# Performance work log

Hardware: AMD Instinct MI355X
Metric: run time of the kernel (lower is better)

The kernel has to match this reference:

```python
import jax, jax.numpy as jnp
import numpy as np

B, S, D, H = 4, 1024, 1024, 16
DH = D // H
EPS = 1e-5


def setup_inputs() -> dict:
    key = jax.random.key(0)
    ks = jax.random.split(key, 8)
    return {
        "q": jax.random.normal(ks[0], (B, S, D), jnp.float32),
        "k": jax.random.normal(ks[1], (B, S, D), jnp.float32),
        "v": jax.random.normal(ks[2], (B, S, D), jnp.float32),
        "mask": jnp.ones((B, S), jnp.float32),
        "scores": jax.random.normal(ks[3], (B, H, S, S), jnp.float32),
        "W_proj": jax.random.normal(ks[4], (D, D), jnp.float32) / np.sqrt(D),
        "W_minus": jax.random.normal(ks[5], (D, 2 * D), jnp.float32) / np.sqrt(2 * D),
        "ln_w": jnp.ones((D,), jnp.float32),
        "ln_b": jnp.zeros((D,), jnp.float32),
        "c": jnp.zeros((1,), jnp.float32),
    }


def reference(q, k, v, mask, scores, W_proj, W_minus, ln_w, ln_b, c):
    # split heads: (B,S,D) -> (B,S,H,DH)
    qh = q.reshape(B, S, H, DH)
    kh = k.reshape(B, S, H, DH)
    vh = v.reshape(B, S, H, DH)
    # scaled QK^T plus learnable-scaled residual scores
    att_scores = jnp.einsum("bqhd,bkhd->bhqk", qh, kh) / np.sqrt(DH) + c[0] * scores
    # additive mask (mask is (B, kv_len))
    att_scores = att_scores - 1e8 * (1.0 - mask)[:, None, None, :]
    att = jax.nn.softmax(att_scores, axis=-1)
    ctx = jnp.einsum("bhqk,bkhd->bqhd", att, vh).reshape(B, S, D)
    # proj (bias-free linear); dropout is identity at inference
    x = ctx @ W_proj.T
    # concat -> minus linear -> LayerNorm
    cat = jnp.concatenate([q, x], axis=-1)
    y = cat @ W_minus.T
    mu = jnp.mean(y, axis=-1, keepdims=True)
    var = jnp.mean((y - mu) ** 2, axis=-1, keepdims=True)
    y = (y - mu) * jax.lax.rsqrt(var + EPS) * ln_w + ln_b
    return (y, att_scores)
```

## Files before the change

kernel.cpp:

```cpp
#include <hip/hip_runtime.h>
#include <hip/hip_bf16.h>
#include <math.h>

#define BB 4
#define SS 1024
#define DD 1024
#define HH 16
#define DHH 64
#define BHH (BB * HH)

#define LDB 88
#define LDC 68

typedef __attribute__((ext_vector_type(8))) short short8;
typedef __attribute__((ext_vector_type(4))) float f32x4;

__device__ __forceinline__ unsigned short f2bf(float x) {
  __hip_bfloat16 h = __float2bfloat16(x);
  return *reinterpret_cast<unsigned short*>(&h);
}

__device__ __forceinline__ void stageb(const unsigned short* __restrict__ src, int ld,
                                       unsigned short* __restrict__ dst, int tid) {
#pragma unroll
  for (int u = 0; u < 2; ++u) {
    int cidx = tid + 256 * u;
    int r = cidx >> 3;
    int c8 = (cidx & 7) * 8;
    float4 v = *reinterpret_cast<const float4*>(src + (size_t)r * ld + c8);
    *reinterpret_cast<float4*>(dst + r * LDB + c8) = v;
  }
}

__device__ __forceinline__ short8 ldfrag(const unsigned short* __restrict__ base,
                                         int row16, int kh, int lane) {
  const unsigned short* p = base + (size_t)(row16 + (lane & 15)) * LDB + kh + (lane >> 4) * 8;
  return *reinterpret_cast<const short8*>(p);
}

__device__ __forceinline__ void mfma_tile(const unsigned short* As, const unsigned short* Bs,
                                          int w, int lane, f32x4 acc[4]) {
#pragma unroll
  for (int kh = 0; kh < 64; kh += 32) {
    short8 b = ldfrag(Bs, w * 16, kh, lane);
#pragma unroll
    for (int mb = 0; mb < 4; ++mb) {
      short8 a = ldfrag(As, mb * 16, kh, lane);
      acc[mb] = __builtin_amdgcn_mfma_f32_16x16x32_bf16(a, b, acc[mb], 0, 0, 0);
    }
  }
}

__device__ __forceinline__ void acc_to_lds(float* Cs, const f32x4 acc[4], int w, int lane,
                                           float scale) {
  int quad = lane >> 4, col = w * 16 + (lane & 15);
#pragma unroll
  for (int mb = 0; mb < 4; ++mb)
#pragma unroll
    for (int r = 0; r < 4; ++r)
      Cs[(mb * 16 + quad * 4 + r) * LDC + col] = acc[mb][r] * scale;
}

__global__ __launch_bounds__(256) void cvt_kernel(const float* __restrict__ in,
                                                  unsigned short* __restrict__ out, int n4) {
  int i = blockIdx.x * 256 + threadIdx.x;
  if (i < n4) {
    float4 v = reinterpret_cast<const float4*>(in)[i];
    ushort4 o;
    o.x = f2bf(v.x); o.y = f2bf(v.y); o.z = f2bf(v.z); o.w = f2bf(v.w);
    reinterpret_cast<ushort4*>(out)[i] = o;
  }
}

__global__ __launch_bounds__(256) void vtrans_kernel(const float* __restrict__ v,
                                                     unsigned short* __restrict__ vT) {
  __shared__ unsigned short T[64 * LDC];
  int tid = threadIdx.x;
  int s0 = blockIdx.x * 64, bh = blockIdx.y;
  int b = bh >> 4, h = bh & 15;
#pragma unroll
  for (int u = 0; u < 4; ++u) {
    int f = tid + 256 * u;
    int r = f >> 4, c4 = (f & 15) * 4;
    float4 vv = *reinterpret_cast<const float4*>(v + ((size_t)(b * SS + s0 + r)) * DD + h * DHH + c4);
    T[(c4 + 0) * LDC + r] = f2bf(vv.x);
    T[(c4 + 1) * LDC + r] = f2bf(vv.y);
    T[(c4 + 2) * LDC + r] = f2bf(vv.z);
    T[(c4 + 3) * LDC + r] = f2bf(vv.w);
  }
  __syncthreads();
#pragma unroll
  for (int u = 0; u < 4; ++u) {
    int f = tid + 256 * u;
    int d = f >> 4, s4 = (f & 15) * 4;
    ushort4 o = *reinterpret_cast<const ushort4*>(&T[d * LDC + s4]);
    *reinterpret_cast<ushort4*>(vT + ((size_t)(bh * DHH + d)) * SS + s0 + s4) = o;
  }
}

__global__ __launch_bounds__(256) void attn_fused_kernel(
    const unsigned short* __restrict__ qb, const unsigned short* __restrict__ kb,
    const unsigned short* __restrict__ vT, const float* __restrict__ scores,
    const float* __restrict__ mask, const float* __restrict__ c,
    float* __restrict__ att, unsigned short* __restrict__ ctxb) {
  __shared__ unsigned short Ps[64 * LDB];
  __shared__ unsigned short Ks[64 * LDB];
  __shared__ unsigned short Vs[64 * LDB];
  __shared__ float Cs[64 * LDC];
  __shared__ float mrun[64], lrun[64], ascale[64];
  int tid = threadIdx.x, lane = tid & 63, w = tid >> 6;

  int flat = blockIdx.x + 16 * blockIdx.y;
  int bh = (flat & 7) * 8 + ((flat >> 3) & 7);
  int qt = flat >> 6;
  int b = bh >> 4, h = bh & 15;
  int qr0 = qt * 64;

  int r0 = tid >> 3, c80 = (tid & 7) * 8;
  int r1 = r0 + 32;
  const unsigned short* kB = kb + (size_t)b * SS * DD + h * DHH;
  const unsigned short* vB = vT + (size_t)bh * DHH * SS;
  unsigned short* KsW0 = Ks + r0 * LDB + c80;
  unsigned short* KsW1 = Ks + r1 * LDB + c80;
  unsigned short* VsW0 = Vs + r0 * LDB + c80;
  unsigned short* VsW1 = Vs + r1 * LDB + c80;

  int rowe = tid >> 4;
  int c4 = (tid & 15) * 4;
  size_t eOff = ((size_t)(bh * SS + qr0 + rowe)) * SS + c4;
  size_t mkOff = (size_t)b * SS + c4;

  stageb(qb + ((size_t)(b * SS + qr0)) * DD + h * DHH, DD, Ps, tid);
  {
    float4 k0 = *reinterpret_cast<const float4*>(kB + (size_t)r0 * DD + c80);
    float4 k1 = *reinterpret_cast<const float4*>(kB + (size_t)r1 * DD + c80);
    float4 v0 = *reinterpret_cast<const float4*>(vB + (size_t)r0 * SS + c80);
    float4 v1 = *reinterpret_cast<const float4*>(vB + (size_t)r1 * SS + c80);
    *reinterpret_cast<float4*>(KsW0) = k0;
    *reinterpret_cast<float4*>(KsW1) = k1;
    *reinterpret_cast<float4*>(VsW0) = v0;
    *reinterpret_cast<float4*>(VsW1) = v1;
  }
  if (tid < 64) { mrun[tid] = -3.0e38f; lrun[tid] = 0.0f; }

  float4 sc[4];
#pragma unroll
  for (int u2 = 0; u2 < 4; ++u2)
    sc[u2] = *reinterpret_cast<const float4*>(scores + eOff + (size_t)u2 * 16 * SS);
  float4 mk = *reinterpret_cast<const float4*>(mask + mkOff);

  __syncthreads();

  short8 qa[2][4];
#pragma unroll
  for (int kh = 0; kh < 2; ++kh)
#pragma unroll
    for (int mb = 0; mb < 4; ++mb)
      qa[kh][mb] = ldfrag(Ps, mb * 16, kh * 32, lane);

  float cc = c[0];
  f32x4 accO[4] = {};

  for (int kt = 0; kt < 16; ++kt) {
    int kr0 = kt * 64;
    float4 kn0 = {}, kn1 = {}, vn0 = {}, vn1 = {};
    if (kt < 15) {
      int kr = kr0 + 64;
      kn0 = *reinterpret_cast<const float4*>(kB + (size_t)(kr + r0) * DD + c80);
      kn1 = *reinterpret_cast<const float4*>(kB + (size_t)(kr + r1) * DD + c80);
      vn0 = *reinterpret_cast<const float4*>(vB + (size_t)r0 * SS + kr + c80);
      vn1 = *reinterpret_cast<const float4*>(vB + (size_t)r1 * SS + kr + c80);
    }

    f32x4 acc[4] = {};
    __builtin_amdgcn_s_setprio(1);
#pragma unroll
    for (int kh = 0; kh < 2; ++kh) {
      short8 bfr = ldfrag(Ks, w * 16, kh * 32, lane);
#pragma unroll
      for (int mb = 0; mb < 4; ++mb)
        acc[mb] = __builtin_amdgcn_mfma_f32_16x16x32_bf16(qa[kh][mb], bfr, acc[mb], 0, 0, 0);
    }
    __builtin_amdgcn_s_setprio(0);
    acc_to_lds(Cs, acc, w, lane, 0.125f);
    __syncthreads();

#pragma unroll
    for (int u2 = 0; u2 < 4; ++u2) {
      int row = rowe + 16 * u2;
      float4 qk = *reinterpret_cast<const float4*>(&Cs[row * LDC + c4]);
      float o0 = qk.x + cc * sc[u2].x - 1e8f * (1.0f - mk.x);
      float o1 = qk.y + cc * sc[u2].y - 1e8f * (1.0f - mk.y);
      float o2 = qk.z + cc * sc[u2].z - 1e8f * (1.0f - mk.z);
      float o3 = qk.w + cc * sc[u2].w - 1e8f * (1.0f - mk.w);
      float4 ov = {o0, o1, o2, o3};
      *reinterpret_cast<float4*>(att + eOff + (size_t)u2 * 16 * SS + kr0) = ov;
      float m = fmaxf(fmaxf(o0, o1), fmaxf(o2, o3));
#pragma unroll
      for (int off = 1; off <= 8; off <<= 1) m = fmaxf(m, __shfl_xor(m, off));
      float mo = mrun[row];
      float mn = fmaxf(mo, m);
      float e0 = __expf(o0 - mn), e1 = __expf(o1 - mn);
      float e2 = __expf(o2 - mn), e3 = __expf(o3 - mn);
      float l = e0 + e1 + e2 + e3;
#pragma unroll
      for (int off = 1; off <= 8; off <<= 1) l += __shfl_xor(l, off);
      ushort4 pv;
      pv.x = f2bf(e0); pv.y = f2bf(e1); pv.z = f2bf(e2); pv.w = f2bf(e3);
      *reinterpret_cast<ushort4*>(&Ps[row * LDB + c4]) = pv;
      if ((tid & 15) == 0) {
        float a = __expf(mo - mn);
        lrun[row] = lrun[row] * a + l;
        mrun[row] = mn;
        ascale[row] = a;
      }
    }
    if (kt < 15) {
#pragma unroll
      for (int u2 = 0; u2 < 4; ++u2)
        sc[u2] = *reinterpret_cast<const float4*>(scores + eOff + (size_t)u2 * 16 * SS + kr0 + 64);
      mk = *reinterpret_cast<const float4*>(mask + mkOff + kr0 + 64);
    }
    __syncthreads();

#pragma unroll
    for (int mb = 0; mb < 4; ++mb) {
      int rb = mb * 16 + (lane >> 4) * 4;
      accO[mb][0] *= ascale[rb + 0];
      accO[mb][1] *= ascale[rb + 1];
      accO[mb][2] *= ascale[rb + 2];
      accO[mb][3] *= ascale[rb + 3];
    }
    __builtin_amdgcn_s_setprio(1);
    mfma_tile(Ps, Vs, w, lane, accO);
    __builtin_amdgcn_s_setprio(0);
    __syncthreads();
    if (kt < 15) {
      *reinterpret_cast<float4*>(KsW0) = kn0;
      *reinterpret_cast<float4*>(KsW1) = kn1;
      *reinterpret_cast<float4*>(VsW0) = vn0;
      *reinterpret_cast<float4*>(VsW1) = vn1;
      __syncthreads();
    }
  }

#pragma unroll
  for (int mb = 0; mb < 4; ++mb) {
    int rb = mb * 16 + (lane >> 4) * 4;
    accO[mb][0] *= 1.0f / lrun[rb + 0];
    accO[mb][1] *= 1.0f / lrun[rb + 1];
    accO[mb][2] *= 1.0f / lrun[rb + 2];
    accO[mb][3] *= 1.0f / lrun[rb + 3];
  }
  acc_to_lds(Cs, accO, w, lane, 1.0f);
  __syncthreads();
#pragma unroll
  for (int u = 0; u < 4; ++u) {
    int f = tid + 256 * u;
    int row = f >> 4, cc4 = (f & 15) * 4;
    float4 vv = *reinterpret_cast<const float4*>(&Cs[row * LDC + cc4]);
    ushort4 o;
    o.x = f2bf(vv.x); o.y = f2bf(vv.y); o.z = f2bf(vv.z); o.w = f2bf(vv.w);
    *reinterpret_cast<ushort4*>(ctxb + ((size_t)(b * SS + qr0 + row)) * DD + h * DHH + cc4) = o;
  }
}

__global__ __launch_bounds__(256) void proj_mfma_kernel(
    const unsigned short* __restrict__ A, const unsigned short* __restrict__ W,
    unsigned short* __restrict__ X) {
  __shared__ unsigned short smem[2 * 64 * LDB];
  unsigned short* As = smem;
  unsigned short* Bs = smem + 64 * LDB;
  float* Cs = reinterpret_cast<float*>(smem);
  int tid = threadIdx.x, lane = tid & 63, w = tid >> 6;
  int d0 = blockIdx.x * 64, n0 = blockIdx.y * 64;
  f32x4 acc[4] = {};
  for (int kc = 0; kc < DD; kc += 64) {
    stageb(A + (size_t)n0 * DD + kc, DD, As, tid);
    stageb(W + (size_t)d0 * DD + kc, DD, Bs, tid);
    __syncthreads();
    mfma_tile(As, Bs, w, lane, acc);
    __syncthreads();
  }
  acc_to_lds(Cs, acc, w, lane, 1.0f);
  __syncthreads();
#pragma unroll
  for (int u = 0; u < 4; ++u) {
    int f = tid + 256 * u;
    int row = f >> 4, c4 = (f & 15) * 4;
    float4 vv = *reinterpret_cast<const float4*>(&Cs[row * LDC + c4]);
    ushort4 o;
    o.x = f2bf(vv.x); o.y = f2bf(vv.y); o.z = f2bf(vv.z); o.w = f2bf(vv.w);
    *reinterpret_cast<ushort4*>(X + (size_t)(n0 + row) * DD + d0 + c4) = o;
  }
}

__global__ __launch_bounds__(256) void minus_mfma_kernel(
    const unsigned short* __restrict__ qb, const unsigned short* __restrict__ xb,
    const unsigned short* __restrict__ Wm, float* __restrict__ Y) {
  __shared__ unsigned short smem[2 * 64 * LDB];
  unsigned short* As = smem;
  unsigned short* Bs = smem + 64 * LDB;
  float* Cs = reinterpret_cast<float*>(smem);
  int tid = threadIdx.x, lane = tid & 63, w = tid >> 6;
  int d0 = blockIdx.x * 64, n0 = blockIdx.y * 64;
  f32x4 acc[4] = {};
  for (int kc = 0; kc < 2 * DD; kc += 64) {
    const unsigned short* asrc = (kc < DD) ? (qb + (size_t)n0 * DD + kc)
                                           : (xb + (size_t)n0 * DD + (kc - DD));
    stageb(asrc, DD, As, tid);
    stageb(Wm + (size_t)d0 * (2 * DD) + kc, 2 * DD, Bs, tid);
    __syncthreads();
    mfma_tile(As, Bs, w, lane, acc);
    __syncthreads();
  }
  acc_to_lds(Cs, acc, w, lane, 1.0f);
  __syncthreads();
#pragma unroll
  for (int u = 0; u < 4; ++u) {
    int f = tid + 256 * u;
    int row = f >> 4, c4 = (f & 15) * 4;
    float4 vv = *reinterpret_cast<const float4*>(&Cs[row * LDC + c4]);
    *reinterpret_cast<float4*>(Y + (size_t)(n0 + row) * DD + d0 + c4) = vv;
  }
}

__global__ __launch_bounds__(256) void ln_kernel(
    float* __restrict__ Y, const float* __restrict__ w, const float* __restrict__ b) {
  __shared__ float ps[4], ps2[4];
  int row = blockIdx.x, t = threadIdx.x;
  float* rp = Y + (size_t)row * DD;
  float4 v = *reinterpret_cast<const float4*>(rp + t * 4);
  float s = v.x + v.y + v.z + v.w;
  float s2 = v.x * v.x + v.y * v.y + v.z * v.z + v.w * v.w;
#pragma unroll
  for (int o = 32; o > 0; o >>= 1) {
    s += __shfl_down(s, o);
    s2 += __shfl_down(s2, o);
  }
  if ((t & 63) == 0) { ps[t >> 6] = s; ps2[t >> 6] = s2; }
  __syncthreads();
  s = ps[0] + ps[1] + ps[2] + ps[3];
  s2 = ps2[0] + ps2[1] + ps2[2] + ps2[3];
  float mu = s * (1.0f / DD);
  float var = s2 * (1.0f / DD) - mu * mu;
  float rs = rsqrtf(var + 1e-5f);
  float4 wv = *reinterpret_cast<const float4*>(w + t * 4);
  float4 bv = *reinterpret_cast<const float4*>(b + t * 4);
  float4 ov;
  ov.x = (v.x - mu) * rs * wv.x + bv.x;
  ov.y = (v.y - mu) * rs * wv.y + bv.y;
  ov.z = (v.z - mu) * rs * wv.z + bv.z;
  ov.w = (v.w - mu) * rs * wv.w + bv.w;
  *reinterpret_cast<float4*>(rp + t * 4) = ov;
}

extern "C" void kernel_launch(void* const* d_in, const int* in_sizes, int n_in,
                              void* d_out, int out_size, void* d_ws, size_t ws_size,
                              hipStream_t stream) {
  const float* q      = (const float*)d_in[0];
  const float* k      = (const float*)d_in[1];
  const float* v      = (const float*)d_in[2];
  const float* mask   = (const float*)d_in[3];
  const float* scores = (const float*)d_in[4];
  const float* W_proj = (const float*)d_in[5];
  const float* W_minus= (const float*)d_in[6];
  const float* ln_w   = (const float*)d_in[7];
  const float* ln_b   = (const float*)d_in[8];
  const float* c      = (const float*)d_in[9];

  float* y   = (float*)d_out;
  float* att = y + (size_t)BB * SS * DD;

  const size_t MB = 1u << 20;
  char* w = (char*)d_ws;
  unsigned short* qb   = (unsigned short*)(w);
  unsigned short* kb   = (unsigned short*)(w + 8 * MB);
  unsigned short* vT   = (unsigned short*)(w + 16 * MB);
  unsigned short* Wpb  = (unsigned short*)(w + 24 * MB);
  unsigned short* Wmb  = (unsigned short*)(w + 26 * MB);
  unsigned short* ctxb = (unsigned short*)(w + 30 * MB);
  unsigned short* xb   = (unsigned short*)(w + 38 * MB);

  const int NQ = BB * SS * DD;
  cvt_kernel<<<dim3(NQ / 4 / 256), 256, 0, stream>>>(q, qb, NQ / 4);
  cvt_kernel<<<dim3(NQ / 4 / 256), 256, 0, stream>>>(k, kb, NQ / 4);
  cvt_kernel<<<dim3(DD * DD / 4 / 256), 256, 0, stream>>>(W_proj, Wpb, DD * DD / 4);
  cvt_kernel<<<dim3(2 * DD * DD / 4 / 256), 256, 0, stream>>>(W_minus, Wmb, 2 * DD * DD / 4);
  vtrans_kernel<<<dim3(16, BHH), 256, 0, stream>>>(v, vT);

  attn_fused_kernel<<<dim3(16, BHH), 256, 0, stream>>>(qb, kb, vT, scores, mask, c, att, ctxb);
  proj_mfma_kernel<<<dim3(16, 64), 256, 0, stream>>>(ctxb, Wpb, xb);
  minus_mfma_kernel<<<dim3(16, 64), 256, 0, stream>>>(qb, xb, Wmb, y);
  ln_kernel<<<dim3(BB * SS), 256, 0, stream>>>(y, ln_w, ln_b);
}
```

Measured before the change: 676.2 us.

## Load K/V MFMA fragments directly from global into registers, drop LDS staging

In the fused attention kernel each wave now loads its own K and V B-operand fragments straight from global memory into registers, with one tile of register prefetch, instead of staging K and V tiles through shared memory. This removes the Ks/Vs LDS buffers and the two barriers per key tile that guarded their refill. It also adds a launch-bounds occupancy hint of 4 blocks. In exchange there are more, less-coalesced global loads per wave (16-byte strided reads per lane), higher register pressure, and an added barrier before the final Cs reuse.

```diff
diff --git a/kernel.cpp b/kernel.cpp
--- a/kernel.cpp
+++ b/kernel.cpp
@@ -98,14 +98,12 @@
   }
 }
 
-__global__ __launch_bounds__(256) void attn_fused_kernel(
+__global__ __launch_bounds__(256, 4) void attn_fused_kernel(
     const unsigned short* __restrict__ qb, const unsigned short* __restrict__ kb,
     const unsigned short* __restrict__ vT, const float* __restrict__ scores,
     const float* __restrict__ mask, const float* __restrict__ c,
     float* __restrict__ att, unsigned short* __restrict__ ctxb) {
   __shared__ unsigned short Ps[64 * LDB];
-  __shared__ unsigned short Ks[64 * LDB];
-  __shared__ unsigned short Vs[64 * LDB];
   __shared__ float Cs[64 * LDC];
   __shared__ float mrun[64], lrun[64], ascale[64];
   int tid = threadIdx.x, lane = tid & 63, w = tid >> 6;
@@ -116,14 +114,10 @@
   int b = bh >> 4, h = bh & 15;
   int qr0 = qt * 64;
 
-  int r0 = tid >> 3, c80 = (tid & 7) * 8;
-  int r1 = r0 + 32;
-  const unsigned short* kB = kb + (size_t)b * SS * DD + h * DHH;
-  const unsigned short* vB = vT + (size_t)bh * DHH * SS;
-  unsigned short* KsW0 = Ks + r0 * LDB + c80;
-  unsigned short* KsW1 = Ks + r1 * LDB + c80;
-  unsigned short* VsW0 = Vs + r0 * LDB + c80;
-  unsigned short* VsW1 = Vs + r1 * LDB + c80;
+  const unsigned short* kF = kb + (size_t)b * SS * DD + h * DHH
+                             + (size_t)(w * 16 + (lane & 15)) * DD + (lane >> 4) * 8;
+  const unsigned short* vF = vT + (size_t)bh * DHH * SS
+                             + (size_t)(w * 16 + (lane & 15)) * SS + (lane >> 4) * 8;
 
   int rowe = tid >> 4;
   int c4 = (tid & 15) * 4;
@@ -131,17 +125,13 @@
   size_t mkOff = (size_t)b * SS + c4;
 
   stageb(qb + ((size_t)(b * SS + qr0)) * DD + h * DHH, DD, Ps, tid);
-  {
-    float4 k0 = *reinterpret_cast<const float4*>(kB + (size_t)r0 * DD + c80);
-    float4 k1 = *reinterpret_cast<const float4*>(kB + (size_t)r1 * DD + c80);
-    float4 v0 = *reinterpret_cast<const float4*>(vB + (size_t)r0 * SS + c80);
-    float4 v1 = *reinterpret_cast<const float4*>(vB + (size_t)r1 * SS + c80);
-    *reinterpret_cast<float4*>(KsW0) = k0;
-    *reinterpret_cast<float4*>(KsW1) = k1;
-    *reinterpret_cast<float4*>(VsW0) = v0;
-    *reinterpret_cast<float4*>(VsW1) = v1;
-  }
   if (tid < 64) { mrun[tid] = -3.0e38f; lrun[tid] = 0.0f; }
+
+  short8 kcur[2], vcur[2];
+  kcur[0] = *reinterpret_cast<const short8*>(kF);
+  kcur[1] = *reinterpret_cast<const short8*>(kF + 32);
+  vcur[0] = *reinterpret_cast<const short8*>(vF);
+  vcur[1] = *reinterpret_cast<const short8*>(vF + 32);
 
   float4 sc[4];
 #pragma unroll
@@ -163,24 +153,21 @@
 
   for (int kt = 0; kt < 16; ++kt) {
     int kr0 = kt * 64;
-    float4 kn0 = {}, kn1 = {}, vn0 = {}, vn1 = {};
+    short8 kn[2] = {}, vn[2] = {};
     if (kt < 15) {
-      int kr = kr0 + 64;
-      kn0 = *reinterpret_cast<const float4*>(kB + (size_t)(kr + r0) * DD + c80);
-      kn1 = *reinterpret_cast<const float4*>(kB + (size_t)(kr + r1) * DD + c80);
-      vn0 = *reinterpret_cast<const float4*>(vB + (size_t)r0 * SS + kr + c80);
-      vn1 = *reinterpret_cast<const float4*>(vB + (size_t)r1 * SS + kr + c80);
+      kn[0] = *reinterpret_cast<const short8*>(kF + (size_t)(kr0 + 64) * DD);
+      kn[1] = *reinterpret_cast<const short8*>(kF + (size_t)(kr0 + 64) * DD + 32);
+      vn[0] = *reinterpret_cast<const short8*>(vF + kr0 + 64);
+      vn[1] = *reinterpret_cast<const short8*>(vF + kr0 + 64 + 32);
     }
 
     f32x4 acc[4] = {};
     __builtin_amdgcn_s_setprio(1);
 #pragma unroll
-    for (int kh = 0; kh < 2; ++kh) {
-      short8 bfr = ldfrag(Ks, w * 16, kh * 32, lane);
+    for (int kh = 0; kh < 2; ++kh)
 #pragma unroll
       for (int mb = 0; mb < 4; ++mb)
-        acc[mb] = __builtin_amdgcn_mfma_f32_16x16x32_bf16(qa[kh][mb], bfr, acc[mb], 0, 0, 0);
-    }
+        acc[mb] = __builtin_amdgcn_mfma_f32_16x16x32_bf16(qa[kh][mb], kcur[kh], acc[mb], 0, 0, 0);
     __builtin_amdgcn_s_setprio(0);
     acc_to_lds(Cs, acc, w, lane, 0.125f);
     __syncthreads();
@@ -232,16 +219,16 @@
       accO[mb][3] *= ascale[rb + 3];
     }
     __builtin_amdgcn_s_setprio(1);
-    mfma_tile(Ps, Vs, w, lane, accO);
+#pragma unroll
+    for (int kh = 0; kh < 2; ++kh)
+#pragma unroll
+      for (int mb = 0; mb < 4; ++mb) {
+        short8 pa = ldfrag(Ps, mb * 16, kh * 32, lane);
+        accO[mb] = __builtin_amdgcn_mfma_f32_16x16x32_bf16(pa, vcur[kh], accO[mb], 0, 0, 0);
+      }
     __builtin_amdgcn_s_setprio(0);
-    __syncthreads();
-    if (kt < 15) {
-      *reinterpret_cast<float4*>(KsW0) = kn0;
-      *reinterpret_cast<float4*>(KsW1) = kn1;
-      *reinterpret_cast<float4*>(VsW0) = vn0;
-      *reinterpret_cast<float4*>(VsW1) = vn1;
-      __syncthreads();
-    }
+    kcur[0] = kn[0]; kcur[1] = kn[1];
+    vcur[0] = vn[0]; vcur[1] = vn[1];
   }
 
 #pragma unroll
@@ -252,6 +239,7 @@
     accO[mb][2] *= 1.0f / lrun[rb + 2];
     accO[mb][3] *= 1.0f / lrun[rb + 3];
   }
+  __syncthreads();
   acc_to_lds(Cs, accO, w, lane, 1.0f);
   __syncthreads();
 #pragma unroll
```

Result: slower. 715.1 us (+5.8%).
